# Kernel tuning notes

Measured on AMD Instinct MI355X. Metric: run time of the kernel, lower is better.

## Reference

```python
import jax, jax.numpy as jnp
import numpy as np

EMBD_DIM = 512
HIDDEN_DIM = 512
TARGET_DIM = 128
BATCH = 64
MAX_SET = 2048


def setup_inputs() -> dict:
    key = jax.random.key(0)
    ks = jax.random.split(key, 10)
    E, H, T = EMBD_DIM, HIDDEN_DIM, TARGET_DIM
    s = lambda fan_in: 1.0 / np.sqrt(fan_in)
    return {
        "words": jax.random.normal(ks[0], (BATCH, MAX_SET, E), dtype=jnp.float32),
        # attention_layer: Linear(2E -> H) followed by tanh; v: (H, 1)
        "W_att": jax.random.uniform(ks[1], (2 * E, H), jnp.float32, -s(2 * E), s(2 * E)),
        "b_att": jax.random.uniform(ks[2], (H,), jnp.float32, -s(2 * E), s(2 * E)),
        "v": jax.random.normal(ks[3], (H, 1), dtype=jnp.float32),
        # pred_net: Linear(E,H) -> ReLU -> Linear(H,H) -> ReLU -> Linear(H,T)
        "W1": jax.random.uniform(ks[4], (E, H), jnp.float32, -s(E), s(E)),
        "b1": jax.random.uniform(ks[5], (H,), jnp.float32, -s(E), s(E)),
        "W2": jax.random.uniform(ks[6], (H, H), jnp.float32, -s(H), s(H)),
        "b2": jax.random.uniform(ks[7], (H,), jnp.float32, -s(H), s(H)),
        "W3": jax.random.uniform(ks[8], (H, T), jnp.float32, -s(H), s(H)),
        "b3": jax.random.uniform(ks[9], (T,), jnp.float32, -s(H), s(H)),
    }


def reference(words, W_att, b_att, v, W1, b1, W2, b2, W3, b3):
    # words: [B, S, E]. A row is "valid" iff its feature-sum is nonzero
    # (matches words.sum(2).abs().sign() in the torch code).
    mask = jnp.sign(jnp.abs(words.sum(-1)))           # [B, S], 0/1 float
    lengths = mask.sum(axis=1, keepdims=True)          # [B, 1]
    # context = mean over valid rows (padded rows are exactly zero)
    context = words.sum(axis=1, keepdims=True) / lengths[..., None]  # [B, 1, E]
    context = jnp.broadcast_to(context, words.shape)   # [B, S, E]

    x = jnp.concatenate([words, context], axis=-1)     # [B, S, 2E]
    h = jnp.tanh(x @ W_att + b_att)                    # [B, S, H]
    scores = (h @ v)[..., 0]                           # [B, S]

    # per-segment softmax over valid rows only (masked_select + per-batch
    # Softmax in the original == masked softmax here)
    scores = jnp.where(mask > 0, scores, jnp.full_like(scores, -1e30))
    attn = jax.nn.softmax(scores, axis=1)              # [B, S]

    rep = jnp.einsum("bs,bse->be", attn, words)        # [B, E]

    pred = jax.nn.relu(rep @ W1 + b1)
    pred = jax.nn.relu(pred @ W2 + b2)
    pred = pred @ W3 + b3                              # [B, T]
    return pred
```

## Files before the change

kernel.cpp:

```cpp
#include <hip/hip_runtime.h>
#include <hip/hip_bf16.h>
#include <hip/hip_fp16.h>
#include <math.h>

#define B 64
#define S 2048
#define E 512
#define HD 512
#define TD 128
#define M_TOT (B*S)

#define OFF_MASK   0
#define OFF_CTXP   (OFF_MASK + B*S)
#define OFF_LENP   (OFF_CTXP + 8*B*E)
#define OFF_CB     (OFF_LENP + 8*B)
#define OFF_REPP   (OFF_CB + B*HD)
#define OFF_SCP    (OFF_REPP + 8*B*E)
#define OFF_WPK    (OFF_SCP + 4*B*S)

typedef __attribute__((ext_vector_type(8))) short short8;
typedef __attribute__((ext_vector_type(4))) float f32x4;

__device__ inline unsigned int f2hu(float x) {
    __half h = __float2half(x);
    unsigned short u; __builtin_memcpy(&u, &h, 2); return (unsigned int)u;
}

__device__ inline float fast_tanh(float x) {
    float a = fabsf(x);
    float e = __expf(-2.0f * a);
    float r = (1.0f - e) / (1.0f + e);
    return copysignf(r, x);
}

__global__ __launch_bounds__(256)
void k0_pack(const float* __restrict__ W_att, unsigned short* __restrict__ Wpk)
{
    int tid = blockIdx.x*256 + threadIdx.x;
    int e = tid >> 9, h = tid & 511;
    float w = W_att[(size_t)e*HD + h];
    int kstep = e >> 5, kb = (e >> 3) & 3, j = e & 7, f = h >> 4, l15 = h & 15;
    size_t dst = ((((size_t)kstep*32 + f)*64) + kb*16 + l15)*8 + j;
    Wpk[dst] = (unsigned short)f2hu(w);
}

__global__ __launch_bounds__(256)
void k1_maskcol(const float* __restrict__ words, float* __restrict__ mask,
                float* __restrict__ ctxp, float* __restrict__ lenp)
{
    int bid = blockIdx.x;
    int b = bid >> 3, ch = bid & 7;
    int t = threadIdx.x;
    int w = t >> 6, l = t & 63;
    __shared__ __align__(16) float colred[4][E];
    __shared__ float lenred[4];
    const float* base = words + (size_t)(b * S + ch * 256) * E;
    float4 c0 = make_float4(0.f,0.f,0.f,0.f), c1 = make_float4(0.f,0.f,0.f,0.f);
    float wlen = 0.0f;
    for (int r = w; r < 256; r += 4) {
        const float* row = base + (size_t)r * E;
        float4 a  = *(const float4*)(row + 4*l);
        float4 bb = *(const float4*)(row + 256 + 4*l);
        float rs = a.x+a.y+a.z+a.w + bb.x+bb.y+bb.z+bb.w;
        #pragma unroll
        for (int m = 1; m < 64; m <<= 1) rs += __shfl_xor(rs, m);
        c0.x += a.x;  c0.y += a.y;  c0.z += a.z;  c0.w += a.w;
        c1.x += bb.x; c1.y += bb.y; c1.z += bb.z; c1.w += bb.w;
        if (l == 0) {
            float mv = (rs != 0.0f) ? 1.0f : 0.0f;
            mask[(size_t)b*S + ch*256 + r] = mv;
            wlen += mv;
        }
    }
    *(float4*)&colred[w][4*l]       = c0;
    *(float4*)&colred[w][256 + 4*l] = c1;
    if (l == 0) lenred[w] = wlen;
    __syncthreads();
    float s1 = colred[0][t]+colred[1][t]+colred[2][t]+colred[3][t];
    float s2 = colred[0][t+256]+colred[1][t+256]+colred[2][t+256]+colred[3][t+256];
    size_t o = ((size_t)ch * B + b) * E;
    ctxp[o + t]       = s1;
    ctxp[o + t + 256] = s2;
    if (t == 0) lenp[ch*B + b] = lenred[0]+lenred[1]+lenred[2]+lenred[3];
}

__global__ __launch_bounds__(256)
void k2_cb(const float* __restrict__ W_att, const float* __restrict__ b_att,
           const float* __restrict__ ctxp, const float* __restrict__ lenp,
           float* __restrict__ cb)
{
    int bid = blockIdx.x;
    int b = bid >> 1, hc = bid & 1;
    int t = threadIdx.x;
    __shared__ float ctxL[E];
    float len = 0.f;
    #pragma unroll
    for (int k = 0; k < 8; ++k) len += lenp[k*B + b];
    float inv = 1.0f / len;
    for (int c = t; c < E; c += 256) {
        float sv = 0.f;
        #pragma unroll
        for (int k = 0; k < 8; ++k) sv += ctxp[((size_t)k*B + b)*E + c];
        ctxL[c] = sv * inv;
    }
    __syncthreads();
    int h = hc*256 + t;
    const float* Wb = W_att + (size_t)E * HD;
    float a0 = b_att[h], a1 = 0.f, a2 = 0.f, a3 = 0.f;
    #pragma unroll 4
    for (int e = 0; e < E; e += 4) {
        a0 += ctxL[e]   * Wb[(size_t)e*HD + h];
        a1 += ctxL[e+1] * Wb[(size_t)(e+1)*HD + h];
        a2 += ctxL[e+2] * Wb[(size_t)(e+2)*HD + h];
        a3 += ctxL[e+3] * Wb[(size_t)(e+3)*HD + h];
    }
    cb[(size_t)b*HD + h] = (a0 + a1) + (a2 + a3);
}

__global__ __launch_bounds__(512, 4)
void k3_scores(const float* __restrict__ words,
               const unsigned short* __restrict__ Wpk,
               const float* __restrict__ cb, const float* __restrict__ v,
               float* __restrict__ scp)
{
    __shared__ __align__(16) unsigned char smem[16384];
    int bid = blockIdx.x;
    int mt = bid >> 2, nc = bid & 3;
    int m0 = mt * 128;
    int b  = m0 >> 11;
    int t = threadIdx.x;
    int lane = t & 63, wid = t >> 6;
    int wr = wid >> 2, wc = wid & 3;

    f32x4 acc[4][2];
    #pragma unroll
    for (int i = 0; i < 4; ++i)
        #pragma unroll
        for (int j = 0; j < 2; ++j) acc[i][j] = (f32x4)0.0f;

    int r = t >> 2, kq = t & 3;
    const float* aSrc = words + (size_t)(m0 + r)*E + kq*8;
    int abase = (r >> 4)*1024 + kq*256 + (r & 15)*16;

    const unsigned short* bBase = Wpk + (((size_t)(nc*8 + wc*2))*64 + lane)*8;
#define LDB(ks,cf) (*(const short8*)(bBase + ((size_t)(ks)*32 + (cf))*512))

    float4 R0a, R0b, R1a, R1b, Rta, Rtb;
#define LOADA(Ra, Rb, ks) do { const float* _s = aSrc + (ks)*32; \
        Ra = *(const float4*)(_s); Rb = *(const float4*)(_s + 4); } while(0)
#define STAGEA(buf, Ra, Rb) do { \
        unsigned int u0 = f2hu(Ra.x) | (f2hu(Ra.y) << 16); \
        unsigned int u1 = f2hu(Ra.z) | (f2hu(Ra.w) << 16); \
        unsigned int u2 = f2hu(Rb.x) | (f2hu(Rb.y) << 16); \
        unsigned int u3 = f2hu(Rb.z) | (f2hu(Rb.w) << 16); \
        *(uint4*)&(buf)[abase] = make_uint4(u0, u1, u2, u3); } while(0)

    unsigned char* sm0 = smem;
    unsigned char* sm1 = smem + 8192;

    LOADA(Rta, Rtb, 0);
    STAGEA(sm0, Rta, Rtb);
    LOADA(R1a, R1b, 1);
    LOADA(R0a, R0b, 2);
    short8 bE[2], bO[2];
    bE[0] = LDB(0, 0); bE[1] = LDB(0, 1);
    bO[0] = LDB(1, 0); bO[1] = LDB(1, 1);
    __syncthreads();

#define KBODY(k, BUFC, BUFN, RSa, RSb, BF) do { \
        short8 ah[4]; \
        _Pragma("unroll") \
        for (int rf = 0; rf < 4; ++rf) \
            ah[rf] = *(const short8*)&(BUFC)[(wr*4 + rf)*1024 + lane*16]; \
        if ((k) < 15) STAGEA(BUFN, RSa, RSb); \
        if ((k) < 13) LOADA(RSa, RSb, (k) + 3); \
        _Pragma("unroll") \
        for (int cf = 0; cf < 2; ++cf) { \
            _Pragma("unroll") \
            for (int rf = 0; rf < 4; ++rf) \
                acc[rf][cf] = __builtin_amdgcn_mfma_f32_16x16x32_f16(ah[rf], BF[cf], acc[rf][cf], 0, 0, 0); \
            if ((k) < 14) BF[cf] = LDB((k) + 2, cf); \
        } \
        __syncthreads(); } while(0)

    #pragma unroll
    for (int kk = 0; kk < 8; ++kk) {
        KBODY(2*kk,     sm0, sm1, R1a, R1b, bE);
        KBODY(2*kk + 1, sm1, sm0, R0a, R0b, bO);
    }
#undef KBODY
#undef LOADA
#undef STAGEA
#undef LDB

    float ssum[4][4];
    #pragma unroll
    for (int i = 0; i < 4; ++i)
        #pragma unroll
        for (int rr = 0; rr < 4; ++rr) ssum[i][rr] = 0.f;

    #pragma unroll
    for (int cf = 0; cf < 2; ++cf) {
        int col = nc*128 + wc*32 + cf*16 + (lane & 15);
        float cbv = cb[(size_t)b*HD + col];
        float vv  = v[col];
        #pragma unroll
        for (int rf = 0; rf < 4; ++rf)
            #pragma unroll
            for (int rr = 0; rr < 4; ++rr)
                ssum[rf][rr] += fast_tanh(acc[rf][cf][rr] + cbv) * vv;
    }
    #pragma unroll
    for (int m = 1; m < 16; m <<= 1)
        #pragma unroll
        for (int rf = 0; rf < 4; ++rf)
            #pragma unroll
            for (int rr = 0; rr < 4; ++rr)
                ssum[rf][rr] += __shfl_xor(ssum[rf][rr], m);

    float* scr = (float*)smem;
    if ((lane & 15) == 0) {
        #pragma unroll
        for (int rf = 0; rf < 4; ++rf)
            #pragma unroll
            for (int rr = 0; rr < 4; ++rr)
                scr[wc*128 + wr*64 + rf*16 + (lane >> 4)*4 + rr] = ssum[rf][rr];
    }
    __syncthreads();
    if (t < 128) {
        float val = (scr[t] + scr[128 + t]) + (scr[256 + t] + scr[384 + t]);
        scp[(size_t)nc*M_TOT + m0 + t] = val;
    }
}

__global__ __launch_bounds__(256)
void k4_rep(const float* __restrict__ words, const float* __restrict__ scp,
            const float* __restrict__ mask, float* __restrict__ repp)
{
    int bid = blockIdx.x;
    int b = bid >> 3, ch = bid & 7;
    int t = threadIdx.x;
    __shared__ float red[256];
    __shared__ float wrow[256];

    float xs[8];
    float mx = -1e30f;
    #pragma unroll
    for (int k = 0; k < 8; ++k) {
        size_t m = (size_t)b*S + 256*k + t;
        float x = (scp[m] + scp[(size_t)M_TOT + m])
                + (scp[(size_t)2*M_TOT + m] + scp[(size_t)3*M_TOT + m]);
        x = (mask[m] > 0.0f) ? x : -1e30f;
        xs[k] = x; mx = fmaxf(mx, x);
    }
    red[t] = mx; __syncthreads();
    for (int off = 128; off > 0; off >>= 1) {
        if (t < off) red[t] = fmaxf(red[t], red[t+off]);
        __syncthreads();
    }
    float gmax = red[0]; __syncthreads();
    float se = 0.f;
    #pragma unroll
    for (int k = 0; k < 8; ++k) se += expf(xs[k] - gmax);
    red[t] = se; __syncthreads();
    for (int off = 128; off > 0; off >>= 1) {
        if (t < off) red[t] += red[t+off];
        __syncthreads();
    }
    float den = red[0];
    wrow[t] = expf(xs[ch] - gmax) / den;
    __syncthreads();

    const float* base = words + (size_t)(b*S + ch*256)*E + 2*t;
    float2 acc = make_float2(0.f, 0.f);
    #pragma unroll 4
    for (int rr = 0; rr < 256; ++rr) {
        float2 wv = *(const float2*)(base + (size_t)rr*E);
        float a = wrow[rr];
        acc.x = fmaf(a, wv.x, acc.x);
        acc.y = fmaf(a, wv.y, acc.y);
    }
    size_t o = ((size_t)ch*B + b)*E + 2*t;
    *(float2*)&repp[o] = acc;
}

__global__ __launch_bounds__(256)
void k5_mlp(const float* __restrict__ repp,
            const float* __restrict__ W1, const float* __restrict__ b1,
            const float* __restrict__ W2, const float* __restrict__ b2,
            const float* __restrict__ W3, const float* __restrict__ b3,
            float* __restrict__ out)
{
    int b = blockIdx.x;
    int t = threadIdx.x;
    __shared__ float xL[HD];
    __shared__ float yL[HD];
    for (int c = t; c < E; c += 256) {
        float sv = 0.f;
        #pragma unroll
        for (int k = 0; k < 8; ++k) sv += repp[((size_t)k*B + b)*E + c];
        xL[c] = sv;
    }
    __syncthreads();
    #pragma unroll
    for (int oo = 0; oo < 2; ++oo) {
        int h = oo*256 + t;
        float a0 = b1[h], a1 = 0.f, a2 = 0.f, a3 = 0.f;
        #pragma unroll 4
        for (int e = 0; e < E; e += 4) {
            a0 += xL[e]   * W1[(size_t)e*HD + h];
            a1 += xL[e+1] * W1[(size_t)(e+1)*HD + h];
            a2 += xL[e+2] * W1[(size_t)(e+2)*HD + h];
            a3 += xL[e+3] * W1[(size_t)(e+3)*HD + h];
        }
        yL[h] = fmaxf((a0 + a1) + (a2 + a3), 0.f);
    }
    __syncthreads();
    float l2v[2];
    #pragma unroll
    for (int oo = 0; oo < 2; ++oo) {
        int h = oo*256 + t;
        float a0 = b2[h], a1 = 0.f, a2 = 0.f, a3 = 0.f;
        #pragma unroll 4
        for (int e = 0; e < HD; e += 4) {
            a0 += yL[e]   * W2[(size_t)e*HD + h];
            a1 += yL[e+1] * W2[(size_t)(e+1)*HD + h];
            a2 += yL[e+2] * W2[(size_t)(e+2)*HD + h];
            a3 += yL[e+3] * W2[(size_t)(e+3)*HD + h];
        }
        l2v[oo] = fmaxf((a0 + a1) + (a2 + a3), 0.f);
    }
    __syncthreads();
    xL[t] = l2v[0]; xL[256 + t] = l2v[1];
    __syncthreads();
    if (t < TD) {
        float a0 = b3[t], a1 = 0.f, a2 = 0.f, a3 = 0.f;
        #pragma unroll 4
        for (int e = 0; e < HD; e += 4) {
            a0 += xL[e]   * W3[(size_t)e*TD + t];
            a1 += xL[e+1] * W3[(size_t)(e+1)*TD + t];
            a2 += xL[e+2] * W3[(size_t)(e+2)*TD + t];
            a3 += xL[e+3] * W3[(size_t)(e+3)*TD + t];
        }
        out[(size_t)b*TD + t] = (a0 + a1) + (a2 + a3);
    }
}

extern "C" void kernel_launch(void* const* d_in, const int* in_sizes, int n_in,
                              void* d_out, int out_size, void* d_ws, size_t ws_size,
                              hipStream_t stream)
{
    const float* words = (const float*)d_in[0];
    const float* W_att = (const float*)d_in[1];
    const float* b_att = (const float*)d_in[2];
    const float* v     = (const float*)d_in[3];
    const float* W1    = (const float*)d_in[4];
    const float* b1    = (const float*)d_in[5];
    const float* W2    = (const float*)d_in[6];
    const float* b2    = (const float*)d_in[7];
    const float* W3    = (const float*)d_in[8];
    const float* b3    = (const float*)d_in[9];
    (void)in_sizes; (void)n_in; (void)out_size; (void)ws_size;

    float* ws   = (float*)d_ws;
    float* mask = ws + OFF_MASK;
    float* ctxp = ws + OFF_CTXP;
    float* lenp = ws + OFF_LENP;
    float* cb   = ws + OFF_CB;
    float* repp = ws + OFF_REPP;
    float* scp  = ws + OFF_SCP;
    unsigned short* Wpk = (unsigned short*)(ws + OFF_WPK);
    float* out  = (float*)d_out;

    hipLaunchKernelGGL(k0_pack,    dim3(1024), dim3(256), 0, stream, W_att, Wpk);
    hipLaunchKernelGGL(k1_maskcol, dim3(B*8),  dim3(256), 0, stream, words, mask, ctxp, lenp);
    hipLaunchKernelGGL(k2_cb,      dim3(B*2),  dim3(256), 0, stream, W_att, b_att, ctxp, lenp, cb);
    hipLaunchKernelGGL(k3_scores,  dim3(4096), dim3(512), 0, stream, words, Wpk, cb, v, scp);
    hipLaunchKernelGGL(k4_rep,     dim3(B*8),  dim3(256), 0, stream, words, scp, mask, repp);
    hipLaunchKernelGGL(k5_mlp,     dim3(B),    dim3(256), 0, stream, repp, W1, b1, W2, b2, W3, b3, out);
}
```

Baseline: 360.8 us.

## Compute full hidden width per score block to stop re-reading words four times

The scores GEMM now uses 64-row tiles that each cover all 512 hidden columns, replacing 128-row tiles split across four column chunks. Each block reads its words rows once instead of four blocks each re-reading and re-converting them. The partial-score buffer and the four-way sum in the softmax kernel go away, and the fp16 A staging layout and k-step schedule are reworked to fit. In exchange each wave holds more accumulators and B fragments, so occupancy drops (launch bounds lowered to 3), and each block streams the whole packed weight matrix.

```diff
diff --git a/kernel.cpp b/kernel.cpp
--- a/kernel.cpp
+++ b/kernel.cpp
@@ -15,8 +15,8 @@
 #define OFF_LENP   (OFF_CTXP + 8*B*E)
 #define OFF_CB     (OFF_LENP + 8*B)
 #define OFF_REPP   (OFF_CB + B*HD)
-#define OFF_SCP    (OFF_REPP + 8*B*E)
-#define OFF_WPK    (OFF_SCP + 4*B*S)
+#define OFF_SC     (OFF_REPP + 8*B*E)
+#define OFF_WPK    (OFF_SC + B*S)
 
 typedef __attribute__((ext_vector_type(8))) short short8;
 typedef __attribute__((ext_vector_type(4))) float f32x4;
@@ -117,95 +117,101 @@
     cb[(size_t)b*HD + h] = (a0 + a1) + (a2 + a3);
 }
 
-__global__ __launch_bounds__(512, 4)
+__global__ __launch_bounds__(512, 3)
 void k3_scores(const float* __restrict__ words,
                const unsigned short* __restrict__ Wpk,
                const float* __restrict__ cb, const float* __restrict__ v,
-               float* __restrict__ scp)
+               float* __restrict__ sc)
 {
     __shared__ __align__(16) unsigned char smem[16384];
-    int bid = blockIdx.x;
-    int mt = bid >> 2, nc = bid & 3;
-    int m0 = mt * 128;
+    int mt = blockIdx.x;
+    int m0 = mt * 64;
     int b  = m0 >> 11;
     int t = threadIdx.x;
     int lane = t & 63, wid = t >> 6;
     int wr = wid >> 2, wc = wid & 3;
 
-    f32x4 acc[4][2];
-    #pragma unroll
-    for (int i = 0; i < 4; ++i)
-        #pragma unroll
-        for (int j = 0; j < 2; ++j) acc[i][j] = (f32x4)0.0f;
-
-    int r = t >> 2, kq = t & 3;
-    const float* aSrc = words + (size_t)(m0 + r)*E + kq*8;
-    int abase = (r >> 4)*1024 + kq*256 + (r & 15)*16;
-
-    const unsigned short* bBase = Wpk + (((size_t)(nc*8 + wc*2))*64 + lane)*8;
-#define LDB(ks,cf) (*(const short8*)(bBase + ((size_t)(ks)*32 + (cf))*512))
-
-    float4 R0a, R0b, R1a, R1b, Rta, Rtb;
-#define LOADA(Ra, Rb, ks) do { const float* _s = aSrc + (ks)*32; \
-        Ra = *(const float4*)(_s); Rb = *(const float4*)(_s + 4); } while(0)
-#define STAGEA(buf, Ra, Rb) do { \
-        unsigned int u0 = f2hu(Ra.x) | (f2hu(Ra.y) << 16); \
-        unsigned int u1 = f2hu(Ra.z) | (f2hu(Ra.w) << 16); \
-        unsigned int u2 = f2hu(Rb.x) | (f2hu(Rb.y) << 16); \
-        unsigned int u3 = f2hu(Rb.z) | (f2hu(Rb.w) << 16); \
-        *(uint4*)&(buf)[abase] = make_uint4(u0, u1, u2, u3); } while(0)
+    f32x4 acc[2][8];
+    #pragma unroll
+    for (int i = 0; i < 2; ++i)
+        #pragma unroll
+        for (int j = 0; j < 8; ++j) acc[i][j] = (f32x4)0.0f;
+
+    {
+    }
+    int sks = t >> 8, sF = (t >> 6) & 3, skb = (t >> 4) & 3, sl15 = t & 15;
+    int srow = sF*16 + sl15;
+    const float* aSrc = words + (size_t)(m0 + srow)*E + sks*32 + skb*8;
+
+    const unsigned short* bBase = Wpk + (((size_t)(wc*8))*64 + lane)*8;
+#define LDB(kst,cf) (*(const short8*)(bBase + ((size_t)(kst)*32 + (cf))*512))
+
+    float4 pa0, pa1, qa0, qa1;
+#define LOADA(P0, P1, s) do { const float* _s = aSrc + (s)*64; \
+        P0 = *(const float4*)(_s); P1 = *(const float4*)(_s + 4); } while(0)
+#define STAGEA(buf, P0, P1) do { \
+        unsigned int u0 = f2hu(P0.x) | (f2hu(P0.y) << 16); \
+        unsigned int u1 = f2hu(P0.z) | (f2hu(P0.w) << 16); \
+        unsigned int u2 = f2hu(P1.x) | (f2hu(P1.y) << 16); \
+        unsigned int u3 = f2hu(P1.z) | (f2hu(P1.w) << 16); \
+        *(uint4*)&(buf)[t*16] = make_uint4(u0, u1, u2, u3); } while(0)
 
     unsigned char* sm0 = smem;
     unsigned char* sm1 = smem + 8192;
 
-    LOADA(Rta, Rtb, 0);
-    STAGEA(sm0, Rta, Rtb);
-    LOADA(R1a, R1b, 1);
-    LOADA(R0a, R0b, 2);
-    short8 bE[2], bO[2];
-    bE[0] = LDB(0, 0); bE[1] = LDB(0, 1);
-    bO[0] = LDB(1, 0); bO[1] = LDB(1, 1);
-    __syncthreads();
-
-#define KBODY(k, BUFC, BUFN, RSa, RSb, BF) do { \
-        short8 ah[4]; \
+    LOADA(pa0, pa1, 0);
+    STAGEA(sm0, pa0, pa1);
+    LOADA(pa0, pa1, 1);
+    LOADA(qa0, qa1, 2);
+    short8 bcur[8];
+    #pragma unroll
+    for (int cf = 0; cf < 8; ++cf) bcur[cf] = LDB(0, cf);
+    __syncthreads();
+
+#define KSUB(kst, BUFC, ksub) do { \
+        short8 ah0 = *(const short8*)&(BUFC)[(ksub)*4096 + (wr*2    )*1024 + lane*16]; \
+        short8 ah1 = *(const short8*)&(BUFC)[(ksub)*4096 + (wr*2 + 1)*1024 + lane*16]; \
         _Pragma("unroll") \
-        for (int rf = 0; rf < 4; ++rf) \
-            ah[rf] = *(const short8*)&(BUFC)[(wr*4 + rf)*1024 + lane*16]; \
-        if ((k) < 15) STAGEA(BUFN, RSa, RSb); \
-        if ((k) < 13) LOADA(RSa, RSb, (k) + 3); \
-        _Pragma("unroll") \
-        for (int cf = 0; cf < 2; ++cf) { \
-            _Pragma("unroll") \
-            for (int rf = 0; rf < 4; ++rf) \
-                acc[rf][cf] = __builtin_amdgcn_mfma_f32_16x16x32_f16(ah[rf], BF[cf], acc[rf][cf], 0, 0, 0); \
-            if ((k) < 14) BF[cf] = LDB((k) + 2, cf); \
-        } \
+        for (int cf = 0; cf < 8; ++cf) { \
+            acc[0][cf] = __builtin_amdgcn_mfma_f32_16x16x32_f16(ah0, bcur[cf], acc[0][cf], 0, 0, 0); \
+            acc[1][cf] = __builtin_amdgcn_mfma_f32_16x16x32_f16(ah1, bcur[cf], acc[1][cf], 0, 0, 0); \
+            if ((kst) < 15) bcur[cf] = LDB((kst) + 1, cf); \
+        } } while(0)
+
+#define SBODY(s, BUFC, BUFN, P0, P1) do { \
+        if ((s) < 7) STAGEA(BUFN, P0, P1); \
+        if ((s) < 5) LOADA(P0, P1, (s) + 3); \
+        KSUB(2*(s),     BUFC, 0); \
+        KSUB(2*(s) + 1, BUFC, 1); \
         __syncthreads(); } while(0)
 
-    #pragma unroll
-    for (int kk = 0; kk < 8; ++kk) {
-        KBODY(2*kk,     sm0, sm1, R1a, R1b, bE);
-        KBODY(2*kk + 1, sm1, sm0, R0a, R0b, bO);
-    }
-#undef KBODY
+    SBODY(0, sm0, sm1, pa0, pa1);
+    SBODY(1, sm1, sm0, qa0, qa1);
+    SBODY(2, sm0, sm1, pa0, pa1);
+    SBODY(3, sm1, sm0, qa0, qa1);
+    SBODY(4, sm0, sm1, pa0, pa1);
+    SBODY(5, sm1, sm0, qa0, qa1);
+    SBODY(6, sm0, sm1, pa0, pa1);
+    SBODY(7, sm1, sm0, qa0, qa1);
+#undef SBODY
+#undef KSUB
 #undef LOADA
 #undef STAGEA
 #undef LDB
 
-    float ssum[4][4];
-    #pragma unroll
-    for (int i = 0; i < 4; ++i)
+    float ssum[2][4];
+    #pragma unroll
+    for (int i = 0; i < 2; ++i)
         #pragma unroll
         for (int rr = 0; rr < 4; ++rr) ssum[i][rr] = 0.f;
 
     #pragma unroll
-    for (int cf = 0; cf < 2; ++cf) {
-        int col = nc*128 + wc*32 + cf*16 + (lane & 15);
+    for (int cf = 0; cf < 8; ++cf) {
+        int col = wc*128 + cf*16 + (lane & 15);
         float cbv = cb[(size_t)b*HD + col];
         float vv  = v[col];
         #pragma unroll
-        for (int rf = 0; rf < 4; ++rf)
+        for (int rf = 0; rf < 2; ++rf)
             #pragma unroll
             for (int rr = 0; rr < 4; ++rr)
                 ssum[rf][rr] += fast_tanh(acc[rf][cf][rr] + cbv) * vv;
@@ -213,7 +219,7 @@
     #pragma unroll
     for (int m = 1; m < 16; m <<= 1)
         #pragma unroll
-        for (int rf = 0; rf < 4; ++rf)
+        for (int rf = 0; rf < 2; ++rf)
             #pragma unroll
             for (int rr = 0; rr < 4; ++rr)
                 ssum[rf][rr] += __shfl_xor(ssum[rf][rr], m);
@@ -221,20 +227,20 @@
     float* scr = (float*)smem;
     if ((lane & 15) == 0) {
         #pragma unroll
-        for (int rf = 0; rf < 4; ++rf)
+        for (int rf = 0; rf < 2; ++rf)
             #pragma unroll
             for (int rr = 0; rr < 4; ++rr)
-                scr[wc*128 + wr*64 + rf*16 + (lane >> 4)*4 + rr] = ssum[rf][rr];
-    }
-    __syncthreads();
-    if (t < 128) {
-        float val = (scr[t] + scr[128 + t]) + (scr[256 + t] + scr[384 + t]);
-        scp[(size_t)nc*M_TOT + m0 + t] = val;
-    }
-}
-
-__global__ __launch_bounds__(256)
-void k4_rep(const float* __restrict__ words, const float* __restrict__ scp,
+                scr[wc*64 + wr*32 + rf*16 + (lane >> 4)*4 + rr] = ssum[rf][rr];
+    }
+    __syncthreads();
+    if (t < 64) {
+        float val = (scr[t] + scr[64 + t]) + (scr[128 + t] + scr[192 + t]);
+        sc[(size_t)m0 + t] = val;
+    }
+}
+
+__global__ __launch_bounds__(256)
+void k4_rep(const float* __restrict__ words, const float* __restrict__ sc,
             const float* __restrict__ mask, float* __restrict__ repp)
 {
     int bid = blockIdx.x;
@@ -248,8 +254,7 @@
     #pragma unroll
     for (int k = 0; k < 8; ++k) {
         size_t m = (size_t)b*S + 256*k + t;
-        float x = (scp[m] + scp[(size_t)M_TOT + m])
-                + (scp[(size_t)2*M_TOT + m] + scp[(size_t)3*M_TOT + m]);
+        float x = sc[m];
         x = (mask[m] > 0.0f) ? x : -1e30f;
         xs[k] = x; mx = fmaxf(mx, x);
     }
@@ -368,14 +373,14 @@
     float* lenp = ws + OFF_LENP;
     float* cb   = ws + OFF_CB;
     float* repp = ws + OFF_REPP;
-    float* scp  = ws + OFF_SCP;
+    float* sc   = ws + OFF_SC;
     unsigned short* Wpk = (unsigned short*)(ws + OFF_WPK);
     float* out  = (float*)d_out;
 
     hipLaunchKernelGGL(k0_pack,    dim3(1024), dim3(256), 0, stream, W_att, Wpk);
     hipLaunchKernelGGL(k1_maskcol, dim3(B*8),  dim3(256), 0, stream, words, mask, ctxp, lenp);
     hipLaunchKernelGGL(k2_cb,      dim3(B*2),  dim3(256), 0, stream, W_att, b_att, ctxp, lenp, cb);
-    hipLaunchKernelGGL(k3_scores,  dim3(4096), dim3(512), 0, stream, words, Wpk, cb, v, scp);
-    hipLaunchKernelGGL(k4_rep,     dim3(B*8),  dim3(256), 0, stream, words, scp, mask, repp);
+    hipLaunchKernelGGL(k3_scores,  dim3(2048), dim3(512), 0, stream, words, Wpk, cb, v, sc);
+    hipLaunchKernelGGL(k4_rep,     dim3(B*8),  dim3(256), 0, stream, words, sc, mask, repp);
     hipLaunchKernelGGL(k5_mlp,     dim3(B),    dim3(256), 0, stream, repp, W1, b1, W2, b2, W3, b3, out);
 }
```

New measurement: 358.7 us. No clear change (-0.6%).
